# Performance work log

Hardware: AMD Instinct MI355X
Metric: run time of the kernel (lower is better)

The kernel has to match this reference:

```python
import jax, jax.numpy as jnp
import numpy as np

N_HEAD = 16

def setup_inputs() -> dict:
    key = jax.random.key(0)
    ks = jax.random.split(key, 5)
    B, T, C = 4, 2048, 1024
    x = jax.random.normal(ks[0], (B, T, C), dtype=jnp.float32)
    # Linear params (torch nn.Linear: y = x @ W.T + b), init scaled like default
    s = 1.0 / np.sqrt(C)
    W_attn = jax.random.uniform(ks[1], (3 * C, C), dtype=jnp.float32, minval=-s, maxval=s)
    b_attn = jax.random.uniform(ks[2], (3 * C,), dtype=jnp.float32, minval=-s, maxval=s)
    W_proj = jax.random.uniform(ks[3], (C, C), dtype=jnp.float32, minval=-s, maxval=s)
    b_proj = jax.random.uniform(ks[4], (C,), dtype=jnp.float32, minval=-s, maxval=s)
    return {"x": x, "W_attn": W_attn, "b_attn": b_attn, "W_proj": W_proj, "b_proj": b_proj}

def reference(x, W_attn, b_attn, W_proj, b_proj):
    B, T, C = x.shape
    H = N_HEAD
    D = C // H
    qkv = jnp.einsum('btc,oc->bto', x, W_attn) + b_attn  # [B,T,3C]
    q, k, v = jnp.split(qkv, 3, axis=2)
    # [B,H,T,D]
    q = q.reshape(B, T, H, D).transpose(0, 2, 1, 3)
    k = k.reshape(B, T, H, D).transpose(0, 2, 1, 3)
    v = v.reshape(B, T, H, D).transpose(0, 2, 1, 3)
    att = jnp.einsum('bhtd,bhsd->bhts', q, k) * (1.0 / np.sqrt(D))  # [B,H,T,T]
    causal = jnp.tril(jnp.ones((T, T), dtype=bool))
    att = jnp.where(causal, att, -jnp.inf)
    att = jax.nn.softmax(att, axis=-1)
    y = jnp.einsum('bhts,bhsd->bhtd', att, v)  # [B,H,T,D]
    y = y.transpose(0, 2, 1, 3).reshape(B, T, C)
    return jnp.einsum('btc,oc->bto', y, W_proj) + b_proj
```

## Files before the change

### kernel.cpp

```cpp
#include <hip/hip_runtime.h>
#include <stdint.h>

typedef unsigned short u16;
typedef __attribute__((ext_vector_type(8))) short short8;
typedef __attribute__((ext_vector_type(4))) float float4v;

#define MFMA16(a, b, c) __builtin_amdgcn_mfma_f32_16x16x32_bf16((a), (b), (c), 0, 0, 0)

#define Q_SCALE 0.18033688011112042f

__device__ __forceinline__ int swz(int row, int col) {
  return row * 64 + (col & 7) + ((((col >> 3) ^ row) & 7) << 3);
}

__device__ __forceinline__ u16 f2b(float f) {
  union { float f; unsigned u; } x; x.f = f;
  unsigned r = x.u + 0x7fffu + ((x.u >> 16) & 1u);
  return (u16)(r >> 16);
}

__device__ __forceinline__ void load_lds_16(const void* g, void* l) {
  __builtin_amdgcn_global_load_lds((__attribute__((address_space(1))) void*)g,
                                   (__attribute__((address_space(3))) void*)l,
                                   16, 0, 0);
}

__global__ __launch_bounds__(256) void cvt_bf16(const float* __restrict__ in,
                                                u16* __restrict__ out, int n8) {
  int i = blockIdx.x * 256 + threadIdx.x;
  if (i >= n8) return;
  const float4* p = (const float4*)in + (size_t)i * 2;
  float4 a = p[0], b = p[1];
  uint4 w;
  w.x = (unsigned)f2b(a.x) | ((unsigned)f2b(a.y) << 16);
  w.y = (unsigned)f2b(a.z) | ((unsigned)f2b(a.w) << 16);
  w.z = (unsigned)f2b(b.x) | ((unsigned)f2b(b.y) << 16);
  w.w = (unsigned)f2b(b.z) | ((unsigned)f2b(b.w) << 16);
  *(uint4*)&out[(size_t)i * 8] = w;
}

__global__ __launch_bounds__(256) void transpose_v(const u16* __restrict__ V,
                                                   u16* __restrict__ Vt) {
  __shared__ u16 tile[64][72];
  const int bh = blockIdx.y;
  const int t0 = blockIdx.x * 64;
  const int tid = threadIdx.x;
  const int r = tid >> 3, c = (tid & 7) * 8;
#pragma unroll
  for (int h = 0; h < 2; ++h) {
    uint4 v = *(const uint4*)&V[((size_t)bh * 2048 + t0 + r + h * 32) * 64 + c];
    const u16* p = (const u16*)&v;
#pragma unroll
    for (int j = 0; j < 8; ++j) tile[c + j][r + h * 32] = p[j];
  }
  __syncthreads();
#pragma unroll
  for (int h = 0; h < 2; ++h) {
    uint4 w;
    u16* p = (u16*)&w;
#pragma unroll
    for (int j = 0; j < 8; ++j) p[j] = tile[r + h * 32][c + j];
    *(uint4*)&Vt[((size_t)bh * 64 + r + h * 32) * 2048 + t0 + c] = w;
  }
}

template <bool QKV_OUT>
__global__ __launch_bounds__(256) void gemm_bt(const u16* __restrict__ A,
                                               const u16* __restrict__ B,
                                               const float* __restrict__ bias,
                                               float* __restrict__ Cf,
                                               u16* __restrict__ QKV,
                                               int M, int N, int K) {
  __shared__ __align__(16) u16 As[128 * 64];
  __shared__ __align__(16) u16 Bs[128 * 64];
  const int tid = threadIdx.x;
  const int lane = tid & 63;
  const int wave = tid >> 6;
  const int quad = lane >> 4;
  const int l15 = lane & 15;
  const int bm0 = blockIdx.y * 128;
  const int bn0 = blockIdx.x * 128;
  const int wm = (wave & 1) * 64;
  const int wn = (wave >> 1) * 64;

  float4v acc[4][4];
#pragma unroll
  for (int i = 0; i < 4; ++i)
#pragma unroll
    for (int j = 0; j < 4; ++j) acc[i][j] = (float4v){0.f, 0.f, 0.f, 0.f};

  const int srow = wave * 32 + (lane >> 3);
  const int scol = ((lane & 7) ^ ((lane >> 3) & 7)) * 8;

  for (int k0 = 0; k0 < K; k0 += 64) {
#pragma unroll
    for (int s = 0; s < 4; ++s) {
      const int r = s * 8;
      load_lds_16(&A[(size_t)(bm0 + srow + r) * K + k0 + scol], &As[(wave * 32 + r) * 64]);
      load_lds_16(&B[(size_t)(bn0 + srow + r) * K + k0 + scol], &Bs[(wave * 32 + r) * 64]);
    }
    __builtin_amdgcn_s_waitcnt(0);
    __syncthreads();
#pragma unroll
    for (int ks = 0; ks < 2; ++ks) {
      short8 af[4], bf[4];
#pragma unroll
      for (int t = 0; t < 4; ++t) {
        af[t] = *(const short8*)&As[swz(wm + t * 16 + l15, ks * 32 + quad * 8)];
        bf[t] = *(const short8*)&Bs[swz(wn + t * 16 + l15, ks * 32 + quad * 8)];
      }
#pragma unroll
      for (int mt = 0; mt < 4; ++mt)
#pragma unroll
        for (int nt = 0; nt < 4; ++nt)
          acc[mt][nt] = MFMA16(af[mt], bf[nt], acc[mt][nt]);
    }
    __syncthreads();
  }

#pragma unroll
  for (int mt = 0; mt < 4; ++mt) {
    const int row0 = bm0 + wm + mt * 16 + quad * 4;
#pragma unroll
    for (int nt = 0; nt < 4; ++nt) {
      const int col = bn0 + wn + nt * 16 + l15;
      const float bs = bias[col];
      if constexpr (QKV_OUT) {
        const int which = col >> 10;
        const int rem = col & 1023;
        const int h = rem >> 6;
        const int d = rem & 63;
        const float sc = (which == 0) ? Q_SCALE : 1.0f;
#pragma unroll
        for (int i = 0; i < 4; ++i) {
          const int t = row0 + i;
          const int b = t >> 11;
          const int tt = t & 2047;
          QKV[(size_t)which * 8388608 +
              ((size_t)(b * 16 + h) * 2048 + tt) * 64 + d] = f2b((acc[mt][nt][i] + bs) * sc);
        }
      } else {
#pragma unroll
        for (int i = 0; i < 4; ++i)
          Cf[(size_t)(row0 + i) * N + col] = acc[mt][nt][i] + bs;
      }
    }
  }
}

__global__ __launch_bounds__(256) void attn_kernel(const u16* __restrict__ QKV,
                                                   const u16* __restrict__ Vt_g,
                                                   u16* __restrict__ Y) {
  const int bx = blockIdx.x;
  const int bh = blockIdx.y;
  const int b = bh >> 4, h = bh & 15;
  const int tid = threadIdx.x;
  const int lane = tid & 63;
  const int wave = tid >> 6;
  const int quad = lane >> 4;
  const int l15 = lane & 15;
  const int qt[2] = {bx, 31 - bx};

  const u16* Qg = QKV + (size_t)bh * 2048 * 64;
  const u16* Kg = QKV + 8388608 + (size_t)bh * 2048 * 64;
  const u16* Vg = Vt_g + (size_t)bh * 64 * 2048;

  __shared__ __align__(16) u16 Ks[2][64 * 64];
  __shared__ __align__(16) u16 Vt[2][64 * 64];
  __shared__ __align__(16) u16 Ps[4][16 * 64];

  short8 qf[2][2];
#pragma unroll
  for (int u = 0; u < 2; ++u)
#pragma unroll
    for (int ks = 0; ks < 2; ++ks)
      qf[u][ks] = *(const short8*)&Qg[(size_t)(qt[u] * 64 + wave * 16 + l15) * 64 + ks * 32 + quad * 8];

  float4v o[2][4];
  float rs[2][4];
#pragma unroll
  for (int u = 0; u < 2; ++u)
#pragma unroll
    for (int i = 0; i < 4; ++i) {
      o[u][i] = (float4v){0.f, 0.f, 0.f, 0.f};
      rs[u][i] = 0.f;
    }

  const int r8 = lane >> 3;
  const int c8 = ((lane & 7) ^ r8) * 8;
  auto stage = [&](int st_, int bufi) {
    const int sb = st_ * 64;
#pragma unroll
    for (int p = 0; p < 2; ++p) {
      const int c = wave * 2 + p;
      load_lds_16(&Kg[(size_t)(sb + c * 8 + r8) * 64 + c8], &Ks[bufi][c * 512]);
      load_lds_16(&Vg[(size_t)(c * 8 + r8) * 2048 + sb + c8], &Vt[bufi][c * 512]);
    }
  };

  const int last = qt[1];
  stage(0, 0);
  __builtin_amdgcn_s_waitcnt(0);
  __syncthreads();

  for (int st = 0; st <= last; ++st) {
    const int cur = st & 1;
    if (st < last) stage(st + 1, cur ^ 1);
    const int sbase = st * 64;
    const bool both = (st <= qt[0]);

    float4v s[2][4];
#pragma unroll
    for (int u = 0; u < 2; ++u)
#pragma unroll
      for (int nt = 0; nt < 4; ++nt) s[u][nt] = (float4v){0.f, 0.f, 0.f, 0.f};
#pragma unroll
    for (int ks = 0; ks < 2; ++ks)
#pragma unroll
      for (int nt = 0; nt < 4; ++nt) {
        const short8 kf = *(const short8*)&Ks[cur][swz(nt * 16 + l15, ks * 32 + quad * 8)];
        s[1][nt] = MFMA16(qf[1][ks], kf, s[1][nt]);
        if (both) s[0][nt] = MFMA16(qf[0][ks], kf, s[0][nt]);
      }

#pragma unroll
    for (int u = 0; u < 2; ++u) {
      if (u == 0 && !both) continue;

      if (st == qt[u]) {
        const int qrow = qt[u] * 64 + wave * 16 + quad * 4;
#pragma unroll
        for (int nt = 0; nt < 4; ++nt) {
          const int kc = sbase + nt * 16 + l15;
#pragma unroll
          for (int i = 0; i < 4; ++i)
            if (kc > qrow + i) s[u][nt][i] = -1e30f;
        }
      }

#pragma unroll
      for (int nt = 0; nt < 4; ++nt)
#pragma unroll
        for (int i = 0; i < 4; ++i) {
          const float p = __builtin_amdgcn_exp2f(s[u][nt][i]);
          s[u][nt][i] = p;
          rs[u][i] += p;
        }

#pragma unroll
      for (int nt = 0; nt < 4; ++nt)
#pragma unroll
        for (int i = 0; i < 4; ++i)
          Ps[wave][swz(quad * 4 + i, nt * 16 + l15)] = f2b(s[u][nt][i]);

#pragma unroll
      for (int ks = 0; ks < 2; ++ks) {
        const short8 pf = *(const short8*)&Ps[wave][swz(l15, ks * 32 + quad * 8)];
#pragma unroll
        for (int dt = 0; dt < 4; ++dt) {
          const short8 vf = *(const short8*)&Vt[cur][swz(dt * 16 + l15, ks * 32 + quad * 8)];
          o[u][dt] = MFMA16(pf, vf, o[u][dt]);
        }
      }
    }

    __builtin_amdgcn_s_waitcnt(0);
    __syncthreads();
  }

#pragma unroll
  for (int u = 0; u < 2; ++u) {
    float linv[4];
#pragma unroll
    for (int i = 0; i < 4; ++i) {
      float r = rs[u][i];
      r += __shfl_xor(r, 1, 16);
      r += __shfl_xor(r, 2, 16);
      r += __shfl_xor(r, 4, 16);
      r += __shfl_xor(r, 8, 16);
      linv[i] = 1.0f / r;
    }
#pragma unroll
    for (int dt = 0; dt < 4; ++dt)
#pragma unroll
      for (int i = 0; i < 4; ++i) {
        const float v = o[u][dt][i] * linv[i];
        const int t = qt[u] * 64 + wave * 16 + quad * 4 + i;
        Y[((size_t)b * 2048 + t) * 1024 + h * 64 + dt * 16 + l15] = f2b(v);
      }
  }
}

extern "C" void kernel_launch(void* const* d_in, const int* in_sizes, int n_in,
                              void* d_out, int out_size, void* d_ws, size_t ws_size,
                              hipStream_t stream) {
  const float* x  = (const float*)d_in[0];
  const float* Wa = (const float*)d_in[1];
  const float* ba = (const float*)d_in[2];
  const float* Wp = (const float*)d_in[3];
  const float* bp = (const float*)d_in[4];
  float* out = (float*)d_out;

  u16* xb  = (u16*)d_ws;
  u16* Wab = xb + 8388608;
  u16* Wpb = Wab + 3145728;
  u16* qkv = Wpb + 1048576;
  u16* y   = xb;
  u16* vt  = (u16*)d_out;

  cvt_bf16<<<4096, 256, 0, stream>>>(x, xb, 1048576);
  cvt_bf16<<<1536, 256, 0, stream>>>(Wa, Wab, 393216);
  cvt_bf16<<<512, 256, 0, stream>>>(Wp, Wpb, 131072);

  gemm_bt<true><<<dim3(24, 64), 256, 0, stream>>>(xb, Wab, ba, nullptr, qkv, 8192, 3072, 1024);
  transpose_v<<<dim3(32, 64), 256, 0, stream>>>(qkv + 16777216, vt);
  attn_kernel<<<dim3(16, 64), 256, 0, stream>>>(qkv, vt, y);
  gemm_bt<false><<<dim3(8, 64), 256, 0, stream>>>(y, Wpb, bp, out, nullptr, 8192, 1024, 1024);
}
```

Measured before the change: 298.1 us.

## Compute softmax row sums via MFMA with ones and interleave PV per k-slice

Replaces the scalar accumulation of softmax denominators and the cross-lane shuffle reduction with an extra MFMA of the bf16 P tile against a vector of ones, so the sums come out already reduced per row. The P staging buffer is split per query tile and per 32-column half with a new swizzle, and the PV MFMAs for both query tiles are interleaved per k-slice. A cheaper round-to-bf16 that drops the tie-to-even step is also used. Denominators are now computed from bf16-rounded probabilities, which matches the numerator's rounding but slightly changes numerics. The extra MFMA adds matrix work.

After: 309.9 us. 1.04x slower.

```diff
diff --git a/kernel.cpp b/kernel.cpp
--- a/kernel.cpp
+++ b/kernel.cpp
@@ -11,12 +11,19 @@
 
 __device__ __forceinline__ int swz(int row, int col) {
   return row * 64 + (col & 7) + ((((col >> 3) ^ row) & 7) << 3);
+}
+__device__ __forceinline__ int swz32(int row, int col) {
+  return row * 32 + (col & 7) + ((((col >> 3) ^ (row >> 1)) & 3) << 3);
 }
 
 __device__ __forceinline__ u16 f2b(float f) {
   union { float f; unsigned u; } x; x.f = f;
   unsigned r = x.u + 0x7fffu + ((x.u >> 16) & 1u);
   return (u16)(r >> 16);
+}
+__device__ __forceinline__ u16 f2b_fast(float f) {
+  union { float f; unsigned u; } x; x.f = f;
+  return (u16)((x.u + 0x8000u) >> 16);
 }
 
 __device__ __forceinline__ void load_lds_16(const void* g, void* l) {
@@ -167,7 +174,11 @@
 
   __shared__ __align__(16) u16 Ks[2][64 * 64];
   __shared__ __align__(16) u16 Vt[2][64 * 64];
-  __shared__ __align__(16) u16 Ps[4][16 * 64];
+  __shared__ __align__(16) u16 Ps[4][2][16 * 32];
+
+  short8 ones;
+#pragma unroll
+  for (int j = 0; j < 8; ++j) ones[j] = (short)0x3F80;
 
   short8 qf[2][2];
 #pragma unroll
@@ -177,14 +188,13 @@
       qf[u][ks] = *(const short8*)&Qg[(size_t)(qt[u] * 64 + wave * 16 + l15) * 64 + ks * 32 + quad * 8];
 
   float4v o[2][4];
-  float rs[2][4];
-#pragma unroll
-  for (int u = 0; u < 2; ++u)
-#pragma unroll
-    for (int i = 0; i < 4; ++i) {
-      o[u][i] = (float4v){0.f, 0.f, 0.f, 0.f};
-      rs[u][i] = 0.f;
-    }
+  float4v osum[2];
+#pragma unroll
+  for (int u = 0; u < 2; ++u) {
+    osum[u] = (float4v){0.f, 0.f, 0.f, 0.f};
+#pragma unroll
+    for (int i = 0; i < 4; ++i) o[u][i] = (float4v){0.f, 0.f, 0.f, 0.f};
+  }
 
   const int r8 = lane >> 3;
   const int c8 = ((lane & 7) ^ r8) * 8;
@@ -226,7 +236,6 @@
 #pragma unroll
     for (int u = 0; u < 2; ++u) {
       if (u == 0 && !both) continue;
-
       if (st == qt[u]) {
         const int qrow = qt[u] * 64 + wave * 16 + quad * 4;
 #pragma unroll
@@ -237,30 +246,34 @@
             if (kc > qrow + i) s[u][nt][i] = -1e30f;
         }
       }
-
 #pragma unroll
       for (int nt = 0; nt < 4; ++nt)
 #pragma unroll
-        for (int i = 0; i < 4; ++i) {
-          const float p = __builtin_amdgcn_exp2f(s[u][nt][i]);
-          s[u][nt][i] = p;
-          rs[u][i] += p;
-        }
-
-#pragma unroll
-      for (int nt = 0; nt < 4; ++nt)
-#pragma unroll
         for (int i = 0; i < 4; ++i)
-          Ps[wave][swz(quad * 4 + i, nt * 16 + l15)] = f2b(s[u][nt][i]);
-
-#pragma unroll
-      for (int ks = 0; ks < 2; ++ks) {
-        const short8 pf = *(const short8*)&Ps[wave][swz(l15, ks * 32 + quad * 8)];
-#pragma unroll
-        for (int dt = 0; dt < 4; ++dt) {
-          const short8 vf = *(const short8*)&Vt[cur][swz(dt * 16 + l15, ks * 32 + quad * 8)];
-          o[u][dt] = MFMA16(pf, vf, o[u][dt]);
-        }
+          s[u][nt][i] = __builtin_amdgcn_exp2f(s[u][nt][i]);
+    }
+
+#pragma unroll
+    for (int ksv = 0; ksv < 2; ++ksv) {
+#pragma unroll
+      for (int u = 0; u < 2; ++u) {
+        if (u == 0 && !both) continue;
+#pragma unroll
+        for (int nh = 0; nh < 2; ++nh)
+#pragma unroll
+          for (int i = 0; i < 4; ++i)
+            Ps[wave][u][swz32(quad * 4 + i, nh * 16 + l15)] = f2b_fast(s[u][2 * ksv + nh][i]);
+      }
+      short8 pf[2];
+      pf[1] = *(const short8*)&Ps[wave][1][swz32(l15, quad * 8)];
+      if (both) pf[0] = *(const short8*)&Ps[wave][0][swz32(l15, quad * 8)];
+      osum[1] = MFMA16(pf[1], ones, osum[1]);
+      if (both) osum[0] = MFMA16(pf[0], ones, osum[0]);
+#pragma unroll
+      for (int dt = 0; dt < 4; ++dt) {
+        const short8 vf = *(const short8*)&Vt[cur][swz(dt * 16 + l15, ksv * 32 + quad * 8)];
+        o[1][dt] = MFMA16(pf[1], vf, o[1][dt]);
+        if (both) o[0][dt] = MFMA16(pf[0], vf, o[0][dt]);
       }
     }
 
@@ -272,14 +285,7 @@
   for (int u = 0; u < 2; ++u) {
     float linv[4];
 #pragma unroll
-    for (int i = 0; i < 4; ++i) {
-      float r = rs[u][i];
-      r += __shfl_xor(r, 1, 16);
-      r += __shfl_xor(r, 2, 16);
-      r += __shfl_xor(r, 4, 16);
-      r += __shfl_xor(r, 8, 16);
-      linv[i] = 1.0f / r;
-    }
+    for (int i = 0; i < 4; ++i) linv[i] = 1.0f / osum[u][i];
 #pragma unroll
     for (int dt = 0; dt < 4; ++dt)
 #pragma unroll
```

## Compute transposed scores so P feeds PV MFMA from registers, skipping LDS

Applied to the files above, without the earlier changes.

Swaps the MFMA operands in QK^T so each lane holds a column of S^T, which matches the A-operand layout of the 16x16x16 bf16 MFMA. The probabilities can then be converted in registers and used directly in the PV product, removing the per-wave Ps shared-memory round trip. The causal mask and row-sum reduction are adjusted for the transposed layout, with final sums exchanged through a small LDS array. A cheaper round-half-up bf16 conversion replaces round-to-nearest-even for P, which can shift numerics slightly, and the PV step now issues twice as many narrower MFMAs.

Result: slower. 316.8 us (+6.3%).

```diff
diff --git a/kernel.cpp b/kernel.cpp
--- a/kernel.cpp
+++ b/kernel.cpp
@@ -3,9 +3,11 @@
 
 typedef unsigned short u16;
 typedef __attribute__((ext_vector_type(8))) short short8;
+typedef __attribute__((ext_vector_type(4))) short short4v;
 typedef __attribute__((ext_vector_type(4))) float float4v;
 
 #define MFMA16(a, b, c) __builtin_amdgcn_mfma_f32_16x16x32_bf16((a), (b), (c), 0, 0, 0)
+#define MFMA16K16(a, b, c) __builtin_amdgcn_mfma_f32_16x16x16bf16_1k((a), (b), (c), 0, 0, 0)
 
 #define Q_SCALE 0.18033688011112042f
 
@@ -17,6 +19,10 @@
   union { float f; unsigned u; } x; x.f = f;
   unsigned r = x.u + 0x7fffu + ((x.u >> 16) & 1u);
   return (u16)(r >> 16);
+}
+__device__ __forceinline__ u16 f2b_fast(float f) {
+  union { float f; unsigned u; } x; x.f = f;
+  return (u16)((x.u + 0x8000u) >> 16);
 }
 
 __device__ __forceinline__ void load_lds_16(const void* g, void* l) {
@@ -161,13 +167,13 @@
   const int l15 = lane & 15;
   const int qt[2] = {bx, 31 - bx};
 
-  const u16* Qg = QKV + (size_t)bh * 2048 * 64;
-  const u16* Kg = QKV + 8388608 + (size_t)bh * 2048 * 64;
-  const u16* Vg = Vt_g + (size_t)bh * 64 * 2048;
+  const u16* Qg = QKV + (size_t)bh * 131072;
+  const u16* Kg = QKV + 8388608 + (size_t)bh * 131072;
+  const u16* Vg = Vt_g + (size_t)bh * 131072;
 
   __shared__ __align__(16) u16 Ks[2][64 * 64];
   __shared__ __align__(16) u16 Vt[2][64 * 64];
-  __shared__ __align__(16) u16 Ps[4][16 * 64];
+  __shared__ float sums[4][2][16];
 
   short8 qf[2][2];
 #pragma unroll
@@ -177,14 +183,11 @@
       qf[u][ks] = *(const short8*)&Qg[(size_t)(qt[u] * 64 + wave * 16 + l15) * 64 + ks * 32 + quad * 8];
 
   float4v o[2][4];
-  float rs[2][4];
+  float rs[2] = {0.f, 0.f};
 #pragma unroll
   for (int u = 0; u < 2; ++u)
 #pragma unroll
-    for (int i = 0; i < 4; ++i) {
-      o[u][i] = (float4v){0.f, 0.f, 0.f, 0.f};
-      rs[u][i] = 0.f;
-    }
+    for (int i = 0; i < 4; ++i) o[u][i] = (float4v){0.f, 0.f, 0.f, 0.f};
 
   const int r8 = lane >> 3;
   const int c8 = ((lane & 7) ^ r8) * 8;
@@ -219,50 +222,44 @@
 #pragma unroll
       for (int nt = 0; nt < 4; ++nt) {
         const short8 kf = *(const short8*)&Ks[cur][swz(nt * 16 + l15, ks * 32 + quad * 8)];
-        s[1][nt] = MFMA16(qf[1][ks], kf, s[1][nt]);
-        if (both) s[0][nt] = MFMA16(qf[0][ks], kf, s[0][nt]);
-      }
-
+        s[1][nt] = MFMA16(kf, qf[1][ks], s[1][nt]);
+        if (both) s[0][nt] = MFMA16(kf, qf[0][ks], s[0][nt]);
+      }
+
+    short4v af[2][4];
 #pragma unroll
     for (int u = 0; u < 2; ++u) {
       if (u == 0 && !both) continue;
-
       if (st == qt[u]) {
-        const int qrow = qt[u] * 64 + wave * 16 + quad * 4;
+        const int qrow = qt[u] * 64 + wave * 16 + l15;
 #pragma unroll
         for (int nt = 0; nt < 4; ++nt) {
-          const int kc = sbase + nt * 16 + l15;
+          const int key0 = sbase + nt * 16 + quad * 4;
 #pragma unroll
           for (int i = 0; i < 4; ++i)
-            if (kc > qrow + i) s[u][nt][i] = -1e30f;
+            if (key0 + i > qrow) s[u][nt][i] = -1e30f;
         }
       }
-
 #pragma unroll
       for (int nt = 0; nt < 4; ++nt)
 #pragma unroll
         for (int i = 0; i < 4; ++i) {
           const float p = __builtin_amdgcn_exp2f(s[u][nt][i]);
-          s[u][nt][i] = p;
-          rs[u][i] += p;
+          rs[u] += p;
+          af[u][nt][i] = (short)f2b_fast(p);
         }
-
-#pragma unroll
-      for (int nt = 0; nt < 4; ++nt)
-#pragma unroll
-        for (int i = 0; i < 4; ++i)
-          Ps[wave][swz(quad * 4 + i, nt * 16 + l15)] = f2b(s[u][nt][i]);
-
-#pragma unroll
-      for (int ks = 0; ks < 2; ++ks) {
-        const short8 pf = *(const short8*)&Ps[wave][swz(l15, ks * 32 + quad * 8)];
-#pragma unroll
-        for (int dt = 0; dt < 4; ++dt) {
-          const short8 vf = *(const short8*)&Vt[cur][swz(dt * 16 + l15, ks * 32 + quad * 8)];
-          o[u][dt] = MFMA16(pf, vf, o[u][dt]);
-        }
-      }
-    }
+    }
+
+#pragma unroll
+    for (int kt = 0; kt < 4; ++kt)
+#pragma unroll
+      for (int dt = 0; dt < 4; ++dt) {
+        const int row = dt * 16 + l15;
+        const int chunk = (kt * 2 + (quad >> 1)) ^ (row & 7);
+        const short4v vf = *(const short4v*)&Vt[cur][row * 64 + chunk * 8 + (quad & 1) * 4];
+        o[1][dt] = MFMA16K16(af[1][kt], vf, o[1][dt]);
+        if (both) o[0][dt] = MFMA16K16(af[0][kt], vf, o[0][dt]);
+      }
 
     __builtin_amdgcn_s_waitcnt(0);
     __syncthreads();
@@ -270,16 +267,16 @@
 
 #pragma unroll
   for (int u = 0; u < 2; ++u) {
+    float r = rs[u];
+    r += __shfl_xor(r, 16, 64);
+    r += __shfl_xor(r, 32, 64);
+    if (quad == 0) sums[wave][u][l15] = r;
+  }
+#pragma unroll
+  for (int u = 0; u < 2; ++u) {
     float linv[4];
 #pragma unroll
-    for (int i = 0; i < 4; ++i) {
-      float r = rs[u][i];
-      r += __shfl_xor(r, 1, 16);
-      r += __shfl_xor(r, 2, 16);
-      r += __shfl_xor(r, 4, 16);
-      r += __shfl_xor(r, 8, 16);
-      linv[i] = 1.0f / r;
-    }
+    for (int i = 0; i < 4; ++i) linv[i] = 1.0f / sums[wave][u][quad * 4 + i];
 #pragma unroll
     for (int dt = 0; dt < 4; ++dt)
 #pragma unroll
```
